# Performance work log

Measured on AMD Instinct MI355X. Metric: run time of the kernel, lower is better.

## Reference

```python
import jax, jax.numpy as jnp
import numpy as np

N_HEAD = 16


def _rope_tables(T, head_dim, dtype):
    # RotaryEmbedding buffers: freqs = outer(t, inv_freq), half-dim tables [T, head_dim//2]
    inv_freq = 1.0 / (10000.0 ** (jnp.arange(0, head_dim, 2, dtype=jnp.float32) / head_dim))
    freqs = jnp.arange(T, dtype=jnp.float32)[:, None] * inv_freq[None, :]
    return jnp.cos(freqs).astype(dtype), jnp.sin(freqs).astype(dtype)


def _apply_rotary(x, cos, sin):
    # x: [B,H,T,D]; cos/sin: [T,D//2] broadcast over B,H
    d = x.shape[-1] // 2
    x1, x2 = x[..., :d], x[..., d:]
    return jnp.concatenate([x1 * cos - x2 * sin, x2 * cos + x1 * sin], axis=-1)


def setup_inputs() -> dict:
    key = jax.random.key(0)
    k1, k2, k3 = jax.random.split(key, 3)
    B, T, C = 2, 2048, 2048
    x = jax.random.normal(k1, (B, T, C), dtype=jnp.float32)
    Wqkv = jax.random.normal(k2, (C, 3 * C), dtype=jnp.float32) * (1.0 / np.sqrt(C))
    Wproj = jax.random.normal(k3, (C, C), dtype=jnp.float32) * (1.0 / np.sqrt(C))
    return {"x": x, "Wqkv": Wqkv, "Wproj": Wproj}


def reference(x, Wqkv, Wproj):
    B, T, C = x.shape
    H = N_HEAD
    D = C // H
    qkv = (x @ Wqkv).reshape(B, T, 3, H, D)
    q, k, v = qkv[:, :, 0], qkv[:, :, 1], qkv[:, :, 2]  # [B,T,H,D]
    q = jnp.transpose(q, (0, 2, 1, 3))  # [B,H,T,D]
    k = jnp.transpose(k, (0, 2, 1, 3))
    v = jnp.transpose(v, (0, 2, 1, 3))
    cos, sin = _rope_tables(T, D, x.dtype)
    q = _apply_rotary(q, cos, sin)
    k = _apply_rotary(k, cos, sin)
    scale = 1.0 / np.sqrt(D)
    scores = jnp.einsum('bhqd,bhkd->bhqk', q, k) * scale
    causal = jnp.tril(jnp.ones((T, T), dtype=bool))
    scores = jnp.where(causal, scores, jnp.finfo(scores.dtype).min)
    attn = jax.nn.softmax(scores, axis=-1)
    out = jnp.einsum('bhqk,bhkd->bhqd', attn, v)
    out = jnp.transpose(out, (0, 2, 1, 3)).reshape(B, T, C)
    return out @ Wproj
```

## Files before the change

### kernel.cpp

```cpp
#include <hip/hip_runtime.h>
#include <hip/hip_bf16.h>

typedef short s16b;
using bf16x4 = __attribute__((ext_vector_type(4))) short;
using bf16x8 = __attribute__((ext_vector_type(8))) short;
using f32x4  = __attribute__((ext_vector_type(4))) float;
using u32x4  = __attribute__((ext_vector_type(4))) unsigned;

#define DEVINL __device__ __forceinline__

DEVINL float bf2f(short u) {
    union { float f; unsigned u; } x;
    x.u = ((unsigned)(unsigned short)u) << 16;
    return x.f;
}
DEVINL short f2bf(float f) {
    unsigned u = __builtin_bit_cast(unsigned, f);
    u += 0x7FFFu + ((u >> 16) & 1u);
    return (short)(u >> 16);
}
DEVINL unsigned cvtpk(float a, float b) {
    unsigned r;
    asm("v_cvt_pk_bf16_f32 %0, %1, %2" : "=v"(r) : "v"(a), "v"(b));
    return r;
}

DEVINL f32x4 mfma16(bf16x8 a, bf16x8 b, f32x4 c) {
    return __builtin_amdgcn_mfma_f32_16x16x32_bf16(a, b, c, 0, 0, 0);
}

DEVINL void gload_lds16(const void* g, void* lds_uniform) {
    __builtin_amdgcn_global_load_lds(
        (const __attribute__((address_space(1))) char*)(const char*)g,
        (__attribute__((address_space(3))) char*)(char*)lds_uniform, 16, 0, 0);
}

DEVINL int perm32(int k) {
    return ((k >> 2) & 3) * 8 + ((k >> 4) & 1) * 4 + (k & 3);
}

DEVINL bf16x8 lds256(const s16b* base, int row, int ds, int g) {
    const char* p = (const char*)base + row * 256 + ((((ds << 2) + g) ^ (row & 7)) << 4);
    return *(const bf16x8*)p;
}

__global__ void k_pre2(const float* __restrict__ x, s16b* __restrict__ xb,
                       float* __restrict__ ctab, float* __restrict__ stab,
                       const float* __restrict__ Wqkv, s16b* __restrict__ wqkvt,
                       const float* __restrict__ Wproj, s16b* __restrict__ wprojt) {
    __shared__ float tile[32][33];
    int bid = blockIdx.x;
    if (bid < 512) {
        int idx = bid * 256 + threadIdx.x;
        int i = idx & 63, t = idx >> 6;
        float inv = powf(10000.0f, -(float)i * (1.0f / 64.0f));
        float fr = (float)t * inv;
        ctab[idx] = cosf(fr);
        stab[idx] = sinf(fr);
    } else if (bid < 8704) {
        int idx = (bid - 512) * 256 + threadIdx.x;
        int p = idx * 4;
        int row = p >> 11, pc = p & 2047;
        int grp = pc >> 5, sp = pc & 31;
        int c = sp >> 3, half = (sp >> 2) & 1;
        int ksrc = grp * 32 + half * 16 + c * 4;
        float4 v = *(const float4*)(x + (size_t)row * 2048 + ksrc);
        bf16x4 o;
        o[0] = f2bf(v.x); o[1] = f2bf(v.y); o[2] = f2bf(v.z); o[3] = f2bf(v.w);
        *(bf16x4*)(xb + (size_t)row * 2048 + pc) = o;
    } else {
        int idx2 = bid - 8704;
        int bx = idx2 & 255, by = idx2 >> 8;
        const float* in; s16b* out; int C, c0;
        if (bx < 192) { in = Wqkv; out = wqkvt; C = 6144; c0 = bx * 32; }
        else          { in = Wproj; out = wprojt; C = 2048; c0 = (bx - 192) * 32; }
        int tx = threadIdx.x & 31, ty = threadIdx.x >> 5;
        int r0 = by * 32;
#pragma unroll
        for (int kk = 0; kk < 4; ++kk) {
            int r = ty + kk * 8;
            tile[r][tx] = in[(size_t)(r0 + r) * C + c0 + tx];
        }
        __syncthreads();
#pragma unroll
        for (int kk = 0; kk < 4; ++kk) {
            int r = ty + kk * 8;
            out[(size_t)(c0 + r) * 2048 + r0 + perm32(tx)] = f2bf(tile[tx][r]);
        }
    }
}

#define STG_B01(DB, KB)                                                        \
  gload_lds16(srcB + (KB), lds + 49152 + (DB) * 32768 + tid16);                \
  gload_lds16(srcB + 262144 + (KB), lds + 49152 + (DB) * 32768 + 8192 + tid16);
#define STG_B23(DB, KB)                                                        \
  gload_lds16(srcB + 524288 + (KB), lds + 49152 + (DB) * 32768 + 16384 + tid16); \
  gload_lds16(srcB + 786432 + (KB), lds + 49152 + (DB) * 32768 + 24576 + tid16);
#define STG_A01(DB, KB)                                                        \
  gload_lds16(srcA + (KB), lds + (DB) * 16384 + tid16);                        \
  gload_lds16(srcA + 262144 + (KB), lds + (DB) * 16384 + 8192 + tid16);

#define AF_READ(B, KS)                                                         \
    _Pragma("unroll")                                                          \
    for (int fi = 0; fi < 4; ++fi) {                                           \
      int row = (fi >> 1) * 64 + wm * 32 + (fi & 1) * 16 + r15;                \
      af[fi] = *(const bf16x8*)(lds + (B) * 16384 + row * 128                  \
               + ((((KS) * 4 + g) ^ (row & 7)) << 4));                         \
    }

#define PH4(B, KH, JH, STGC, WN)                                               \
  {                                                                            \
    if ((JH) == 0) { AF_READ(B, KH) }                                          \
    _Pragma("unroll")                                                          \
    for (int fj = 0; fj < 2; ++fj) {                                           \
      int row = (JH) * 128 + wn * 32 + fj * 16 + r15;                          \
      bfr[fj] = *(const bf16x8*)(lds + 49152 + (B) * 32768 + row * 128         \
                + ((((KH) * 4 + g) ^ (row & 7)) << 4));                        \
    }                                                                          \
    STGC                                                                       \
    if ((WN) == 6) { asm volatile("s_waitcnt vmcnt(6)" ::: "memory");          \
                     __builtin_amdgcn_sched_barrier(0); }                      \
    else if ((WN) == 0) { asm volatile("s_waitcnt vmcnt(0)" ::: "memory");     \
                     __builtin_amdgcn_sched_barrier(0); }                      \
    __builtin_amdgcn_s_barrier();                                              \
    asm volatile("s_waitcnt lgkmcnt(0)" ::: "memory");                         \
    __builtin_amdgcn_sched_barrier(0);                                         \
    __builtin_amdgcn_s_setprio(1);                                             \
    _Pragma("unroll")                                                          \
    for (int fi = 0; fi < 4; ++fi)                                             \
      _Pragma("unroll")                                                        \
      for (int fj = 0; fj < 2; ++fj)                                           \
        acc[fi][(JH) * 2 + fj] = mfma16(af[fi], bfr[fj], acc[fi][(JH) * 2 + fj]); \
    __builtin_amdgcn_s_setprio(0);                                             \
    __builtin_amdgcn_s_barrier();                                              \
    __builtin_amdgcn_sched_barrier(0);                                         \
  }

#define DO_TILE3(B, S1, S2, S3, WNL)                                           \
    PH4(B, 0, 0, S1, -1)                                                       \
    PH4(B, 0, 1, S2, -1)                                                       \
    PH4(B, 1, 0, S3, -1)                                                       \
    PH4(B, 1, 1, , WNL)

#define GEMM3_MAINLOOP(A_, B_)                                                 \
    __shared__ __attribute__((aligned(16))) char lds[147456];                  \
    const int tid = threadIdx.x;                                               \
    const int lane = tid & 63, wave = tid >> 6;                                \
    const int g = lane >> 4, r15 = lane & 15;                                  \
    const int wm = wave >> 2, wn = wave & 3;                                   \
    const int tid16 = tid << 4;                                                \
    const int rowL = tid16 >> 7;                                               \
    const int swzL = ((((tid16 >> 4) & 7) ^ (rowL & 7)) << 4);                 \
    const char* srcA = (const char*)(A_) + (size_t)(bm + rowL) * 4096 + swzL;  \
    const char* srcB = (const char*)(B_) + (size_t)(bn + rowL) * 4096 + swzL;  \
    f32x4 acc[4][4] = {};                                                      \
    bf16x8 af[4], bfr[2];                                                      \
    STG_B01(0, 0) STG_A01(0, 0) STG_B23(0, 0)                                  \
    STG_B01(1, 128) STG_A01(1, 128) STG_B23(1, 128)                            \
    asm volatile("s_waitcnt vmcnt(6)" ::: "memory");                           \
    __builtin_amdgcn_sched_barrier(0);                                         \
    __builtin_amdgcn_s_barrier();                                              \
    for (int t3 = 0; t3 < 10; ++t3) {                                          \
        const int kb2 = (3 * t3 + 2) * 128;                                    \
        const int kb3 = kb2 + 128, kb4 = kb2 + 256;                            \
        DO_TILE3(0, STG_B01(2, kb2), STG_A01(2, kb2), STG_B23(2, kb2), 6)      \
        DO_TILE3(1, STG_B01(0, kb3), STG_A01(0, kb3), STG_B23(0, kb3), 6)      \
        DO_TILE3(2, STG_B01(1, kb4), STG_A01(1, kb4), STG_B23(1, kb4), 6)      \
    }                                                                          \
    DO_TILE3(0, , , , 0)                                                       \
    DO_TILE3(1, , , , -1)

__global__ __launch_bounds__(512) void k_gemm_qkv(
    const s16b* __restrict__ A, const s16b* __restrict__ Bt,
    s16b* __restrict__ Qb, s16b* __restrict__ Kp, s16b* __restrict__ Vt,
    const float* __restrict__ ctab, const float* __restrict__ stab) {
    const int bid = blockIdx.x;
    const int xcd = bid & 7, local = bid >> 3;
    const int rr_ = local >> 5, w = local & 31;
    const int bm = ((xcd & 3) * 8 + (w >> 2)) * 128;
    const int bn = ((xcd >> 2) * 12 + rr_ * 4 + (w & 3)) * 256;
    GEMM3_MAINLOOP(A, Bt)
    const int which = bn >> 11;
    if (which < 2) {
        char* sml = (char*)lds;
#pragma unroll
        for (int i = 0; i < 4; ++i) {
#pragma unroll
            for (int j = 0; j < 4; ++j) {
                int mb0 = (i >> 1) * 64 + wm * 32 + (i & 1) * 16 + 4 * g;
                int nn = (j >> 1) * 128 + wn * 32 + (j & 1) * 16 + r15;
#pragma unroll
                for (int e = 0; e < 4; ++e) {
                    int mm = mb0 + e;
                    *(s16b*)(sml + mm * 528 + ((nn * 2) ^ ((mm & 3) << 5))) =
                        f2bf(acc[i][j][e]);
                }
            }
        }
        __syncthreads();
        const int mrow = tid >> 2, c4 = tid & 3;
        const int bb = bm >> 11;
        const int tt = (bm & 2047) + mrow;
        const char* srow = sml + mrow * 528;
        const int sw = (mrow & 3) << 5;
        bf16x8 v[8];
#pragma unroll
        for (int k = 0; k < 8; ++k) {
            int lc = c4 + 4 * k;
            v[k] = *(const bf16x8*)(srow + ((lc * 16) ^ sw));
        }
        float cs[2][8], sn[2][8];
#pragma unroll
        for (int j = 0; j < 2; ++j) {
            int d0 = 8 * c4 + 32 * j;
            const float* cp = ctab + tt * 64 + d0;
            const float* sp = stab + tt * 64 + d0;
            *(float4*)&cs[j][0] = *(const float4*)cp;
            *(float4*)&cs[j][4] = *(const float4*)(cp + 4);
            *(float4*)&sn[j][0] = *(const float4*)sp;
            *(float4*)&sn[j][4] = *(const float4*)(sp + 4);
        }
        if (which == 0) {
            const float SC = 0.12751744154f;
#pragma unroll
            for (int j = 0; j < 2; ++j)
#pragma unroll
                for (int e = 0; e < 8; ++e) { cs[j][e] *= SC; sn[j][e] *= SC; }
        }
        bf16x8 o[8];
#pragma unroll
        for (int hh = 0; hh < 2; ++hh)
#pragma unroll
            for (int j = 0; j < 2; ++j) {
                int kl = hh * 4 + j, kh = kl + 2;
                bf16x8 r1, r2;
#pragma unroll
                for (int e = 0; e < 8; ++e) {
                    float c = cs[j][e], s = sn[j][e];
                    float x1 = bf2f(v[kl][e]), x2 = bf2f(v[kh][e]);
                    r1[e] = f2bf(x1 * c - x2 * s);
                    r2[e] = f2bf(x2 * c + x1 * s);
                }
                o[kl] = r1; o[kh] = r2;
            }
        if (which == 0) {
#pragma unroll
            for (int k = 0; k < 8; ++k) {
                int lc = c4 + 4 * k;
                int ng = bn + lc * 8;
                int h = (ng >> 7) & 15, d = ng & 127;
                *(bf16x8*)(Qb + ((size_t)(bb * 16 + h) * 2048 + tt) * 128 + d) = o[k];
            }
        } else {
#pragma unroll
            for (int k = 0; k < 8; ++k) {
                int lc = c4 + 4 * k;
                int ng = bn + lc * 8;
                int h = (ng >> 7) & 15, d = ng & 127;
                size_t base = ((size_t)(bb * 16 + h) * 2048 + tt) * 128 + (d & ~31);
                int w2 = d & 31;
                bf16x4 lo, hi;
#pragma unroll
                for (int e = 0; e < 4; ++e) { lo[e] = o[k][e]; hi[e] = o[k][e + 4]; }
                *(bf16x4*)(Kp + base + perm32(w2)) = lo;
                *(bf16x4*)(Kp + base + perm32(w2 + 4)) = hi;
            }
        }
    } else {
#pragma unroll
        for (int i = 0; i < 4; ++i) {
            int m0 = bm + (i >> 1) * 64 + wm * 32 + (i & 1) * 16 + 4 * g;
            int b = m0 >> 11, t0 = m0 & 2047;
            int pt = (t0 & ~31) + perm32(t0 & 31);
#pragma unroll
            for (int j = 0; j < 4; ++j) {
                int n = bn + (j >> 1) * 128 + wn * 32 + (j & 1) * 16 + r15;
                int h = (n >> 7) & 15, d = n & 127;
                size_t base = ((size_t)(b * 16 + h) * 128 + d) * 2048 + pt;
                bf16x4 pk;
#pragma unroll
                for (int e = 0; e < 4; ++e) pk[e] = f2bf(acc[i][j][e]);
                *(bf16x4*)(Vt + base) = pk;
            }
        }
    }
}

__global__ __launch_bounds__(512) void k_gemm_proj(
    const s16b* __restrict__ A, const s16b* __restrict__ Bt, float* __restrict__ Co) {
    const int bid = blockIdx.x;
    const int xcd = bid & 7, local = bid >> 3;
    const int bm = (xcd * 4 + (local & 3)) * 128;
    const int bn = (local >> 2) * 256;
    GEMM3_MAINLOOP(A, Bt)
#pragma unroll
    for (int i = 0; i < 4; ++i) {
        int m0 = bm + (i >> 1) * 64 + wm * 32 + (i & 1) * 16 + 4 * g;
#pragma unroll
        for (int j = 0; j < 4; ++j) {
            int n = bn + (j >> 1) * 128 + wn * 32 + (j & 1) * 16 + r15;
#pragma unroll
            for (int e = 0; e < 4; ++e) Co[(size_t)(m0 + e) * 2048 + n] = acc[i][j][e];
        }
    }
}

__global__ __launch_bounds__(512) void k_attn(
    const s16b* __restrict__ Qb, const s16b* __restrict__ Kp,
    const s16b* __restrict__ Vt, s16b* __restrict__ AO) {
    __shared__ alignas(16) s16b Ks[2][128 * 128];
    __shared__ alignas(16) s16b Vs[2][128 * 128];
    const int tid = threadIdx.x;
    const int lane = tid & 63, wave = tid >> 6;
    const int g = lane >> 4, r15 = lane & 15;
    const int bh = blockIdx.x, pp = blockIdx.y;
    const s16b* Qg = Qb + (size_t)bh * 2048 * 128;
    const char* Kg = (const char*)(Kp + (size_t)bh * 2048 * 128);
    const char* Vg = (const char*)(Vt + (size_t)bh * 128 * 2048);
    const int b = bh >> 4, h = bh & 15;

    const int qt = (wave < 4) ? (15 - pp) : pp;
    const int w2 = wave & 3;
    const int q0 = qt * 128 + w2 * 32;
    const int ktiles = 16 - pp;

#define ASTG(BUF, KT)                                                          \
    {                                                                          \
      const int k0s = (KT) * 128;                                              \
      _Pragma("unroll")                                                        \
      for (int rr = 0; rr < 4; ++rr) {                                         \
        int uo = (rr * 512 + wave * 64) * 16;                                  \
        int o = uo + lane * 16;                                                \
        int row = o >> 8, sl = (o >> 4) & 15;                                  \
        int sg = (sl ^ (row & 7)) << 4;                                        \
        gload_lds16(Kg + (size_t)(k0s + row) * 256 + sg,                       \
                    (char*)Ks + (BUF) * 32768 + uo);                           \
        gload_lds16(Vg + (size_t)row * 4096 + (size_t)k0s * 2 + sg,            \
                    (char*)Vs + (BUF) * 32768 + uo);                           \
      }                                                                        \
    }

    ASTG(0, 0)

    bf16x8 qf[2][4];
#pragma unroll
    for (int qs = 0; qs < 2; ++qs)
#pragma unroll
        for (int ds = 0; ds < 4; ++ds) {
            const s16b* p = Qg + (size_t)(q0 + qs * 16 + r15) * 128 + ds * 32 + 4 * g;
            bf16x4 lo = *(const bf16x4*)p;
            bf16x4 hi = *(const bf16x4*)(p + 16);
            qf[qs][ds] = __builtin_shufflevector(lo, hi, 0, 1, 2, 3, 4, 5, 6, 7);
        }

    f32x4 ot[8][2] = {};
    float m_s[2] = {-3e38f, -3e38f};
    float l_s[2] = {0.f, 0.f};

    for (int kt = 0; kt < ktiles; ++kt) {
        const int k0 = kt * 128;
        if (kt + 1 < ktiles) {
            ASTG((kt + 1) & 1, kt + 1)
            asm volatile("s_waitcnt vmcnt(8)" ::: "memory");
        } else {
            asm volatile("s_waitcnt vmcnt(0)" ::: "memory");
        }
        __builtin_amdgcn_sched_barrier(0);
        __builtin_amdgcn_s_barrier();
        asm volatile("" ::: "memory");
        __builtin_amdgcn_sched_barrier(0);

        if (k0 <= q0 + 31) {
            const s16b* Kb_ = (const s16b*)((const char*)Ks + (kt & 1) * 32768);
            const s16b* Vb_ = (const s16b*)((const char*)Vs + (kt & 1) * 32768);
            f32x4 st[8][2] = {};
            __builtin_amdgcn_s_setprio(1);
#pragma unroll
            for (int ds = 0; ds < 4; ++ds) {
#pragma unroll
                for (int ks = 0; ks < 8; ++ks) {
                    bf16x8 kf = lds256(Kb_, ks * 16 + r15, ds, g);
#pragma unroll
                    for (int qs = 0; qs < 2; ++qs)
                        st[ks][qs] = mfma16(kf, qf[qs][ds], st[ks][qs]);
                }
            }
            __builtin_amdgcn_s_setprio(0);
            if (k0 + 127 > q0) {
#pragma unroll
                for (int ks = 0; ks < 8; ++ks)
#pragma unroll
                    for (int qs = 0; qs < 2; ++qs)
#pragma unroll
                        for (int e = 0; e < 4; ++e) {
                            int kk = k0 + ks * 16 + 4 * g + e;
                            int qq = q0 + qs * 16 + r15;
                            if (kk > qq) st[ks][qs][e] = -3e38f;
                        }
            }
#pragma unroll
            for (int qs = 0; qs < 2; ++qs) {
                float mx = st[0][qs][0];
#pragma unroll
                for (int ks = 0; ks < 8; ++ks)
#pragma unroll
                    for (int e = 0; e < 4; ++e)
                        if (ks | e) mx = fmaxf(mx, st[ks][qs][e]);
                mx = fmaxf(mx, __shfl_xor(mx, 16));
                mx = fmaxf(mx, __shfl_xor(mx, 32));
                if (__any(mx > m_s[qs] + 8.f)) {
                    float mn = fmaxf(m_s[qs], mx);
                    float sf = exp2f(m_s[qs] - mn);
                    m_s[qs] = mn;
                    l_s[qs] *= sf;
#pragma unroll
                    for (int d8 = 0; d8 < 8; ++d8)
#pragma unroll
                        for (int e = 0; e < 4; ++e) ot[d8][qs][e] *= sf;
                }
                float mm = m_s[qs], sum = 0.f;
#pragma unroll
                for (int ks = 0; ks < 8; ++ks)
#pragma unroll
                    for (int e = 0; e < 4; ++e) {
                        float p = exp2f(st[ks][qs][e] - mm);
                        st[ks][qs][e] = p;
                        sum += p;
                    }
                l_s[qs] += sum;
            }
            bf16x8 pb[4][2];
#pragma unroll
            for (int k2 = 0; k2 < 4; ++k2)
#pragma unroll
                for (int qs = 0; qs < 2; ++qs) {
                    u32x4 t;
                    t[0] = cvtpk(st[2 * k2][qs][0], st[2 * k2][qs][1]);
                    t[1] = cvtpk(st[2 * k2][qs][2], st[2 * k2][qs][3]);
                    t[2] = cvtpk(st[2 * k2 + 1][qs][0], st[2 * k2 + 1][qs][1]);
                    t[3] = cvtpk(st[2 * k2 + 1][qs][2], st[2 * k2 + 1][qs][3]);
                    pb[k2][qs] = __builtin_bit_cast(bf16x8, t);
                }
            __builtin_amdgcn_s_setprio(1);
#pragma unroll
            for (int k2 = 0; k2 < 4; ++k2)
#pragma unroll
                for (int d8 = 0; d8 < 8; ++d8) {
                    bf16x8 vf = lds256(Vb_, d8 * 16 + r15, k2, g);
#pragma unroll
                    for (int qs = 0; qs < 2; ++qs)
                        ot[d8][qs] = mfma16(vf, pb[k2][qs], ot[d8][qs]);
                }
            __builtin_amdgcn_s_setprio(0);
        }
        asm volatile("" ::: "memory");
        __builtin_amdgcn_sched_barrier(0);
        __builtin_amdgcn_s_barrier();
    }
#pragma unroll
    for (int qs = 0; qs < 2; ++qs) {
        float l = l_s[qs];
        l += __shfl_xor(l, 16);
        l += __shfl_xor(l, 32);
        float inv = 1.0f / l;
        int q = q0 + qs * 16 + r15;
#pragma unroll
        for (int d8 = 0; d8 < 8; ++d8) {
            uint2 pk2;
            pk2.x = cvtpk(ot[d8][qs][0] * inv, ot[d8][qs][1] * inv);
            pk2.y = cvtpk(ot[d8][qs][2] * inv, ot[d8][qs][3] * inv);
            size_t off = ((size_t)(b * 2048 + q)) * 2048
                       + h * 128 + (d8 >> 1) * 32 + g * 8 + (d8 & 1) * 4;
            *(uint2*)(AO + off) = pk2;
        }
    }
#undef ASTG
}

extern "C" void kernel_launch(void* const* d_in, const int* in_sizes, int n_in,
                              void* d_out, int out_size, void* d_ws, size_t ws_size,
                              hipStream_t stream) {
    const float* x = (const float*)d_in[0];
    const float* Wqkv = (const float*)d_in[1];
    const float* Wproj = (const float*)d_in[2];
    float* out = (float*)d_out;

    char* ws = (char*)d_ws;
    float* ctab = (float*)ws;
    float* stab = ctab + 2048 * 64;
    size_t off = 1048576;
    s16b* xb = (s16b*)(ws + off); off += 16777216;
    s16b* wqkvt = (s16b*)(ws + off); off += 25165824;
    s16b* wprojt = (s16b*)(ws + off); off += 8388608;
    s16b* Qb = (s16b*)(ws + off); off += 16777216;
    s16b* Kp = (s16b*)(ws + off); off += 16777216;
    s16b* Vt = (s16b*)(ws + off); off += 16777216;
    s16b* AO = xb;

    k_pre2<<<dim3(25088), dim3(256), 0, stream>>>(x, xb, ctab, stab,
                                                  Wqkv, wqkvt, Wproj, wprojt);
    k_gemm_qkv<<<dim3(768), dim3(512), 0, stream>>>(xb, wqkvt, Qb, Kp, Vt, ctab, stab);
    k_attn<<<dim3(32, 8), dim3(512), 0, stream>>>(Qb, Kp, Vt, AO);
    k_gemm_proj<<<dim3(256), dim3(512), 0, stream>>>(AO, wprojt, out);
}
```

Baseline: 230.3 us.

## Interleave high and low causal query tiles within each wave for balanced work

Each wave now owns 16 rows from the high query tile and 16 rows from the low tile, instead of four waves taking 32 rows of the high tile and four taking 32 rows of the low tile. All waves therefore stay active over the whole key loop, and the low-tile half is skipped once it passes the causal diagonal. This is meant to remove load imbalance between waves, where low-tile waves used to sit idle at barriers. In exchange it adds branches and duplicated MFMA paths, and each wave does half-width MFMA work on later tiles, which may reduce K/V fragment reuse per LDS read.

```diff
diff --git a/kernel.cpp b/kernel.cpp
--- a/kernel.cpp
+++ b/kernel.cpp
@@ -319,9 +319,8 @@
     const char* Vg = (const char*)(Vt + (size_t)bh * 128 * 2048);
     const int b = bh >> 4, h = bh & 15;
 
-    const int qt = (wave < 4) ? (15 - pp) : pp;
-    const int w2 = wave & 3;
-    const int q0 = qt * 128 + w2 * 32;
+    const int q0h = (15 - pp) * 128 + wave * 16;
+    const int q0l = pp * 128 + wave * 16;
     const int ktiles = 16 - pp;
 
 #define ASTG(BUF, KT)                                                          \
@@ -344,18 +343,62 @@
 
     bf16x8 qf[2][4];
 #pragma unroll
-    for (int qs = 0; qs < 2; ++qs)
+    for (int qs = 0; qs < 2; ++qs) {
+        int q0 = qs ? q0l : q0h;
 #pragma unroll
         for (int ds = 0; ds < 4; ++ds) {
-            const s16b* p = Qg + (size_t)(q0 + qs * 16 + r15) * 128 + ds * 32 + 4 * g;
+            const s16b* p = Qg + (size_t)(q0 + r15) * 128 + ds * 32 + 4 * g;
             bf16x4 lo = *(const bf16x4*)p;
             bf16x4 hi = *(const bf16x4*)(p + 16);
             qf[qs][ds] = __builtin_shufflevector(lo, hi, 0, 1, 2, 3, 4, 5, 6, 7);
         }
+    }
 
     f32x4 ot[8][2] = {};
     float m_s[2] = {-3e38f, -3e38f};
     float l_s[2] = {0.f, 0.f};
+
+#define SMAX(QS)                                                               \
+    {                                                                          \
+        float mx = st[0][QS][0];                                               \
+        _Pragma("unroll")                                                      \
+        for (int ks = 0; ks < 8; ++ks)                                         \
+            _Pragma("unroll")                                                  \
+            for (int e = 0; e < 4; ++e)                                        \
+                if (ks | e) mx = fmaxf(mx, st[ks][QS][e]);                     \
+        mx = fmaxf(mx, __shfl_xor(mx, 16));                                    \
+        mx = fmaxf(mx, __shfl_xor(mx, 32));                                    \
+        if (__any(mx > m_s[QS] + 8.f)) {                                       \
+            float mn = fmaxf(m_s[QS], mx);                                     \
+            float sf = exp2f(m_s[QS] - mn);                                    \
+            m_s[QS] = mn;                                                      \
+            l_s[QS] *= sf;                                                     \
+            _Pragma("unroll")                                                  \
+            for (int d8 = 0; d8 < 8; ++d8)                                     \
+                _Pragma("unroll")                                              \
+                for (int e = 0; e < 4; ++e) ot[d8][QS][e] *= sf;               \
+        }                                                                      \
+        float mm = m_s[QS], sum = 0.f;                                         \
+        _Pragma("unroll")                                                      \
+        for (int ks = 0; ks < 8; ++ks)                                         \
+            _Pragma("unroll")                                                  \
+            for (int e = 0; e < 4; ++e) {                                      \
+                float p = exp2f(st[ks][QS][e] - mm);                           \
+                st[ks][QS][e] = p;                                             \
+                sum += p;                                                      \
+            }                                                                  \
+        l_s[QS] += sum;                                                        \
+    }
+#define PBQ(QS)                                                                \
+    _Pragma("unroll")                                                          \
+    for (int k2 = 0; k2 < 4; ++k2) {                                           \
+        u32x4 t;                                                               \
+        t[0] = cvtpk(st[2 * k2][QS][0], st[2 * k2][QS][1]);                    \
+        t[1] = cvtpk(st[2 * k2][QS][2], st[2 * k2][QS][3]);                    \
+        t[2] = cvtpk(st[2 * k2 + 1][QS][0], st[2 * k2 + 1][QS][1]);            \
+        t[3] = cvtpk(st[2 * k2 + 1][QS][2], st[2 * k2 + 1][QS][3]);            \
+        pb[k2][QS] = __builtin_bit_cast(bf16x8, t);                            \
+    }
 
     for (int kt = 0; kt < ktiles; ++kt) {
         const int k0 = kt * 128;
@@ -370,89 +413,73 @@
         asm volatile("" ::: "memory");
         __builtin_amdgcn_sched_barrier(0);
 
-        if (k0 <= q0 + 31) {
-            const s16b* Kb_ = (const s16b*)((const char*)Ks + (kt & 1) * 32768);
-            const s16b* Vb_ = (const s16b*)((const char*)Vs + (kt & 1) * 32768);
-            f32x4 st[8][2] = {};
-            __builtin_amdgcn_s_setprio(1);
-#pragma unroll
-            for (int ds = 0; ds < 4; ++ds) {
+        const bool lo_act = (k0 <= q0l + 15);
+        const s16b* Kb_ = (const s16b*)((const char*)Ks + (kt & 1) * 32768);
+        const s16b* Vb_ = (const s16b*)((const char*)Vs + (kt & 1) * 32768);
+        f32x4 st[8][2] = {};
+        __builtin_amdgcn_s_setprio(1);
+        if (lo_act) {
+#pragma unroll
+            for (int ds = 0; ds < 4; ++ds)
 #pragma unroll
                 for (int ks = 0; ks < 8; ++ks) {
                     bf16x8 kf = lds256(Kb_, ks * 16 + r15, ds, g);
-#pragma unroll
-                    for (int qs = 0; qs < 2; ++qs)
-                        st[ks][qs] = mfma16(kf, qf[qs][ds], st[ks][qs]);
-                }
-            }
-            __builtin_amdgcn_s_setprio(0);
-            if (k0 + 127 > q0) {
-#pragma unroll
-                for (int ks = 0; ks < 8; ++ks)
-#pragma unroll
-                    for (int qs = 0; qs < 2; ++qs)
-#pragma unroll
-                        for (int e = 0; e < 4; ++e) {
-                            int kk = k0 + ks * 16 + 4 * g + e;
-                            int qq = q0 + qs * 16 + r15;
-                            if (kk > qq) st[ks][qs][e] = -3e38f;
-                        }
-            }
-#pragma unroll
-            for (int qs = 0; qs < 2; ++qs) {
-                float mx = st[0][qs][0];
-#pragma unroll
-                for (int ks = 0; ks < 8; ++ks)
-#pragma unroll
-                    for (int e = 0; e < 4; ++e)
-                        if (ks | e) mx = fmaxf(mx, st[ks][qs][e]);
-                mx = fmaxf(mx, __shfl_xor(mx, 16));
-                mx = fmaxf(mx, __shfl_xor(mx, 32));
-                if (__any(mx > m_s[qs] + 8.f)) {
-                    float mn = fmaxf(m_s[qs], mx);
-                    float sf = exp2f(m_s[qs] - mn);
-                    m_s[qs] = mn;
-                    l_s[qs] *= sf;
-#pragma unroll
-                    for (int d8 = 0; d8 < 8; ++d8)
-#pragma unroll
-                        for (int e = 0; e < 4; ++e) ot[d8][qs][e] *= sf;
-                }
-                float mm = m_s[qs], sum = 0.f;
-#pragma unroll
-                for (int ks = 0; ks < 8; ++ks)
-#pragma unroll
-                    for (int e = 0; e < 4; ++e) {
-                        float p = exp2f(st[ks][qs][e] - mm);
-                        st[ks][qs][e] = p;
-                        sum += p;
-                    }
-                l_s[qs] += sum;
-            }
-            bf16x8 pb[4][2];
-#pragma unroll
-            for (int k2 = 0; k2 < 4; ++k2)
-#pragma unroll
-                for (int qs = 0; qs < 2; ++qs) {
-                    u32x4 t;
-                    t[0] = cvtpk(st[2 * k2][qs][0], st[2 * k2][qs][1]);
-                    t[1] = cvtpk(st[2 * k2][qs][2], st[2 * k2][qs][3]);
-                    t[2] = cvtpk(st[2 * k2 + 1][qs][0], st[2 * k2 + 1][qs][1]);
-                    t[3] = cvtpk(st[2 * k2 + 1][qs][2], st[2 * k2 + 1][qs][3]);
-                    pb[k2][qs] = __builtin_bit_cast(bf16x8, t);
-                }
-            __builtin_amdgcn_s_setprio(1);
+                    st[ks][0] = mfma16(kf, qf[0][ds], st[ks][0]);
+                    st[ks][1] = mfma16(kf, qf[1][ds], st[ks][1]);
+                }
+        } else {
+#pragma unroll
+            for (int ds = 0; ds < 4; ++ds)
+#pragma unroll
+                for (int ks = 0; ks < 8; ++ks) {
+                    bf16x8 kf = lds256(Kb_, ks * 16 + r15, ds, g);
+                    st[ks][0] = mfma16(kf, qf[0][ds], st[ks][0]);
+                }
+        }
+        __builtin_amdgcn_s_setprio(0);
+        if (k0 + 127 > q0h) {
+#pragma unroll
+            for (int ks = 0; ks < 8; ++ks)
+#pragma unroll
+                for (int e = 0; e < 4; ++e) {
+                    int kk = k0 + ks * 16 + 4 * g + e;
+                    if (kk > q0h + r15) st[ks][0][e] = -3e38f;
+                }
+        }
+        if (lo_act && (k0 + 127 > q0l)) {
+#pragma unroll
+            for (int ks = 0; ks < 8; ++ks)
+#pragma unroll
+                for (int e = 0; e < 4; ++e) {
+                    int kk = k0 + ks * 16 + 4 * g + e;
+                    if (kk > q0l + r15) st[ks][1][e] = -3e38f;
+                }
+        }
+        SMAX(0)
+        if (lo_act) { SMAX(1) }
+        bf16x8 pb[4][2];
+        PBQ(0)
+        if (lo_act) { PBQ(1) }
+        __builtin_amdgcn_s_setprio(1);
+        if (lo_act) {
 #pragma unroll
             for (int k2 = 0; k2 < 4; ++k2)
 #pragma unroll
                 for (int d8 = 0; d8 < 8; ++d8) {
                     bf16x8 vf = lds256(Vb_, d8 * 16 + r15, k2, g);
-#pragma unroll
-                    for (int qs = 0; qs < 2; ++qs)
-                        ot[d8][qs] = mfma16(vf, pb[k2][qs], ot[d8][qs]);
-                }
-            __builtin_amdgcn_s_setprio(0);
-        }
+                    ot[d8][0] = mfma16(vf, pb[k2][0], ot[d8][0]);
+                    ot[d8][1] = mfma16(vf, pb[k2][1], ot[d8][1]);
+                }
+        } else {
+#pragma unroll
+            for (int k2 = 0; k2 < 4; ++k2)
+#pragma unroll
+                for (int d8 = 0; d8 < 8; ++d8) {
+                    bf16x8 vf = lds256(Vb_, d8 * 16 + r15, k2, g);
+                    ot[d8][0] = mfma16(vf, pb[k2][0], ot[d8][0]);
+                }
+        }
+        __builtin_amdgcn_s_setprio(0);
         asm volatile("" ::: "memory");
         __builtin_amdgcn_sched_barrier(0);
         __builtin_amdgcn_s_barrier();
@@ -463,7 +490,7 @@
         l += __shfl_xor(l, 16);
         l += __shfl_xor(l, 32);
         float inv = 1.0f / l;
-        int q = q0 + qs * 16 + r15;
+        int q = (qs ? q0l : q0h) + r15;
 #pragma unroll
         for (int d8 = 0; d8 < 8; ++d8) {
             uint2 pk2;
@@ -475,6 +502,8 @@
         }
     }
 #undef ASTG
+#undef SMAX
+#undef PBQ
 }
 
 extern "C" void kernel_launch(void* const* d_in, const int* in_sizes, int n_in,
```

Result: no change. 230.4 us (+0.1%).
